# Optimization experiments

Measured on AMD Instinct MI355X. Metric: run time of the kernel, lower is better.

Reference implementation:

```python
import jax, jax.numpy as jnp
import numpy as np

K = 3  # number of propagation hops (matches init kwarg)
N = 50000
E = 800000
D = 96


def setup_inputs() -> dict:
    key = jax.random.key(0)
    k1, k2, k3, k4 = jax.random.split(key, 4)
    x = jax.random.normal(k1, (N, D), dtype=jnp.float32)
    edge_feature = jax.random.normal(k2, (E, D), dtype=jnp.float32)
    hopwise = jnp.ones((K + 1,), dtype=jnp.float32)  # nn.Parameter(torch.ones(K+1))
    edge_index = jax.random.randint(k3, (2, E), 0, N, dtype=jnp.int64)
    return {"x": x, "edge_feature": edge_feature, "hopwise": hopwise,
            "edge_index": edge_index}


def reference(x, edge_feature, hopwise, edge_index):
    row, col = edge_index[0], edge_index[1]
    n = x.shape[0]
    # degree of destination nodes (col), symmetric normalization
    deg = jax.ops.segment_sum(jnp.ones(col.shape, x.dtype), col, num_segments=n)
    deg_inv = jnp.where(deg > 0, jax.lax.rsqrt(jnp.maximum(deg, 1.0)) * jnp.where(deg > 0, 1.0, 0.0), 0.0)
    deg_inv = jnp.where(deg > 0, deg ** -0.5, 0.0)
    norm = (deg_inv[row] * deg_inv[col])[:, None]  # [E, 1]
    hidden = x * hopwise[0]
    for hop in range(K):
        # message: norm * (x_j + edge_feature); aggregate: scatter-add at col
        msg = norm * (x[row] + edge_feature)          # [E, D]
        x = jax.ops.segment_sum(msg, col, num_segments=n)  # [N, D]
        hidden = hidden + hopwise[hop + 1] * x
    return hidden
```

## Files before the change

### kernel.cpp

```cpp
#include <hip/hip_runtime.h>


#define CH 24
#define CH2 12

typedef float v4f __attribute__((ext_vector_type(4)));

__global__ void deg_kernel(const int* __restrict__ col, int* __restrict__ deg, int E) {
    int e = blockIdx.x * blockDim.x + threadIdx.x;
    if (e < E) atomicAdd(&deg[col[e]], 1);
}

__global__ void deginv_kernel(const int* __restrict__ deg, float* __restrict__ deginv, int n) {
    int i = blockIdx.x * blockDim.x + threadIdx.x;
    if (i < n) {
        int d = deg[i];
        deginv[i] = (d > 0) ? rsqrtf((float)d) : 0.0f;
    }
}

__global__ __launch_bounds__(256) void scan1_kernel(const int* __restrict__ deg,
                                                    int* __restrict__ starts,
                                                    int* __restrict__ bsums, int n) {
    int t = threadIdx.x;
    int i = blockIdx.x * 1024 + t * 4;
    int4 v = make_int4(0, 0, 0, 0);
    if (i + 3 < n) v = *(const int4*)(deg + i);
    else {
        if (i + 0 < n) v.x = deg[i + 0];
        if (i + 1 < n) v.y = deg[i + 1];
        if (i + 2 < n) v.z = deg[i + 2];
        if (i + 3 < n) v.w = deg[i + 3];
    }
    int s0 = v.x, s1 = s0 + v.y, s2 = s1 + v.z, s3 = s2 + v.w;
    int tot = s3;
    int lane = t & 63;
    int incl = tot;
    for (int off = 1; off < 64; off <<= 1) {
        int u = __shfl_up(incl, off, 64);
        if (lane >= off) incl += u;
    }
    __shared__ int wsum[4];
    __shared__ int woff[4];
    int wid = t >> 6;
    if (lane == 63) wsum[wid] = incl;
    __syncthreads();
    if (t == 0) { int a = 0; for (int w = 0; w < 4; ++w) { woff[w] = a; a += wsum[w]; } }
    __syncthreads();
    int excl = incl - tot + woff[wid];
    if (i + 0 < n) starts[i + 0] = excl;
    if (i + 1 < n) starts[i + 1] = excl + s0;
    if (i + 2 < n) starts[i + 2] = excl + s1;
    if (i + 3 < n) starts[i + 3] = excl + s2;
    if (t == 255) bsums[blockIdx.x] = woff[3] + wsum[3];
}

__global__ __launch_bounds__(64) void scan2_kernel(int* __restrict__ bsums, int nb,
                                                   int* __restrict__ starts, int n, int total) {
    int lane = threadIdx.x;
    int v = (lane < nb) ? bsums[lane] : 0;
    int incl = v;
    for (int off = 1; off < 64; off <<= 1) {
        int u = __shfl_up(incl, off, 64);
        if (lane >= off) incl += u;
    }
    if (lane < nb) bsums[lane] = incl - v;
    if (lane == 0) starts[n] = total;
}

__global__ __launch_bounds__(256) void scan3_kernel(int* __restrict__ starts,
                                                    int* __restrict__ cursor,
                                                    const int* __restrict__ bsums, int n) {
    int t = threadIdx.x;
    int i = blockIdx.x * 1024 + t * 4;
    int off = bsums[blockIdx.x];
    for (int k = 0; k < 4; ++k) {
        int ii = i + k;
        if (ii < n) {
            int s = starts[ii] + off;
            starts[ii] = s;
            cursor[ii] = s;
        }
    }
}

__global__ void fill_kernel(const int* __restrict__ col, const int* __restrict__ row,
                            const float* __restrict__ deginv, int* __restrict__ cursor,
                            int* __restrict__ eids, float2* __restrict__ edat, int E) {
    int e = blockIdx.x * blockDim.x + threadIdx.x;
    if (e < E) {
        int c = col[e], r = row[e];
        int pos = atomicAdd(&cursor[c], 1);
        eids[pos] = e;
        float2 o;
        o.x = __int_as_float(r);
        o.y = deginv[r] * deginv[c];
        edat[pos] = o;
    }
}

__global__ __launch_bounds__(256) void hop1_kernel(const int* __restrict__ starts,
                                                   const float2* __restrict__ edat,
                                                   const int* __restrict__ eids,
                                                   const float4* __restrict__ ef4,
                                                   const float4* __restrict__ x4,
                                                   float4* __restrict__ bvec4,
                                                   float4* __restrict__ xnext4,
                                                   float4* __restrict__ out4,
                                                   const float* __restrict__ hopwise,
                                                   int NC2) {
    int g = blockIdx.x * 256 + threadIdx.x;
    if (g >= NC2) return;
    int node = g / CH2;
    int c = g - node * CH2;
    int s = starts[node], e_end = starts[node + 1];
    float4 ab0 = make_float4(0.f, 0.f, 0.f, 0.f), ab1 = ab0;
    float4 ax0 = ab0, ax1 = ab0;
    int j = s;
    for (; j + 2 <= e_end; j += 2) {
        float2 a0 = edat[j], a1 = edat[j + 1];
        int e0 = eids[j], e1 = eids[j + 1];
        int r0 = __float_as_int(a0.x), r1 = __float_as_int(a1.x);
        const v4f* fp0 = (const v4f*)(ef4 + (size_t)e0 * CH + c);
        const v4f* fp1 = (const v4f*)(ef4 + (size_t)e1 * CH + c);
        const float4* xp0 = x4 + (size_t)r0 * CH + c;
        const float4* xp1 = x4 + (size_t)r1 * CH + c;
        v4f f00 = __builtin_nontemporal_load(fp0);
        v4f f01 = __builtin_nontemporal_load(fp0 + 12);
        v4f f10 = __builtin_nontemporal_load(fp1);
        v4f f11 = __builtin_nontemporal_load(fp1 + 12);
        float4 v00 = xp0[0], v01 = xp0[12];
        float4 v10 = xp1[0], v11 = xp1[12];
        ab0.x += a0.y * f00.x + a1.y * f10.x;
        ab0.y += a0.y * f00.y + a1.y * f10.y;
        ab0.z += a0.y * f00.z + a1.y * f10.z;
        ab0.w += a0.y * f00.w + a1.y * f10.w;
        ab1.x += a0.y * f01.x + a1.y * f11.x;
        ab1.y += a0.y * f01.y + a1.y * f11.y;
        ab1.z += a0.y * f01.z + a1.y * f11.z;
        ab1.w += a0.y * f01.w + a1.y * f11.w;
        ax0.x += a0.y * v00.x + a1.y * v10.x;
        ax0.y += a0.y * v00.y + a1.y * v10.y;
        ax0.z += a0.y * v00.z + a1.y * v10.z;
        ax0.w += a0.y * v00.w + a1.y * v10.w;
        ax1.x += a0.y * v01.x + a1.y * v11.x;
        ax1.y += a0.y * v01.y + a1.y * v11.y;
        ax1.z += a0.y * v01.z + a1.y * v11.z;
        ax1.w += a0.y * v01.w + a1.y * v11.w;
    }
    for (; j < e_end; ++j) {
        float2 a = edat[j];
        int e = eids[j];
        int r = __float_as_int(a.x);
        const v4f* fp = (const v4f*)(ef4 + (size_t)e * CH + c);
        const float4* xp = x4 + (size_t)r * CH + c;
        v4f f0 = __builtin_nontemporal_load(fp);
        v4f f1 = __builtin_nontemporal_load(fp + 12);
        float4 v0 = xp[0], v1 = xp[12];
        ab0.x += a.y * f0.x; ab0.y += a.y * f0.y; ab0.z += a.y * f0.z; ab0.w += a.y * f0.w;
        ab1.x += a.y * f1.x; ab1.y += a.y * f1.y; ab1.z += a.y * f1.z; ab1.w += a.y * f1.w;
        ax0.x += a.y * v0.x; ax0.y += a.y * v0.y; ax0.z += a.y * v0.z; ax0.w += a.y * v0.w;
        ax1.x += a.y * v1.x; ax1.y += a.y * v1.y; ax1.z += a.y * v1.z; ax1.w += a.y * v1.w;
    }
    float h0 = hopwise[0], h1 = hopwise[1];
    size_t o = (size_t)node * CH + c;
    float4 xs0 = x4[o], xs1 = x4[o + 12];
    float4 x10, x11;
    x10.x = ax0.x + ab0.x; x10.y = ax0.y + ab0.y; x10.z = ax0.z + ab0.z; x10.w = ax0.w + ab0.w;
    x11.x = ax1.x + ab1.x; x11.y = ax1.y + ab1.y; x11.z = ax1.z + ab1.z; x11.w = ax1.w + ab1.w;
    bvec4[o] = ab0; bvec4[o + 12] = ab1;
    xnext4[o] = x10; xnext4[o + 12] = x11;
    float4 ov0, ov1;
    ov0.x = h0 * xs0.x + h1 * x10.x; ov0.y = h0 * xs0.y + h1 * x10.y;
    ov0.z = h0 * xs0.z + h1 * x10.z; ov0.w = h0 * xs0.w + h1 * x10.w;
    ov1.x = h0 * xs1.x + h1 * x11.x; ov1.y = h0 * xs1.y + h1 * x11.y;
    ov1.z = h0 * xs1.z + h1 * x11.z; ov1.w = h0 * xs1.w + h1 * x11.w;
    out4[o] = ov0; out4[o + 12] = ov1;
}

__global__ __launch_bounds__(256) void hop_kernel(const int* __restrict__ starts,
                                                  const float2* __restrict__ edat,
                                                  const float4* __restrict__ xcur4,
                                                  const float4* __restrict__ bvec4,
                                                  float4* __restrict__ xnext4,
                                                  float4* __restrict__ out4,
                                                  const float* __restrict__ hopwise,
                                                  int hop, int writeNext, int NC2) {
    int g = blockIdx.x * 256 + threadIdx.x;
    if (g >= NC2) return;
    int node = g / CH2;
    int c = g - node * CH2;
    int s = starts[node], e_end = starts[node + 1];
    float4 ax0 = make_float4(0.f, 0.f, 0.f, 0.f), ax1 = ax0;
    int j = s;
    for (; j + 4 <= e_end; j += 4) {
        float2 a0 = edat[j], a1 = edat[j + 1], a2 = edat[j + 2], a3 = edat[j + 3];
        int r0 = __float_as_int(a0.x), r1 = __float_as_int(a1.x);
        int r2 = __float_as_int(a2.x), r3 = __float_as_int(a3.x);
        const float4* p0 = xcur4 + (size_t)r0 * CH + c;
        const float4* p1 = xcur4 + (size_t)r1 * CH + c;
        const float4* p2 = xcur4 + (size_t)r2 * CH + c;
        const float4* p3 = xcur4 + (size_t)r3 * CH + c;
        float4 v00 = p0[0], v01 = p0[12];
        float4 v10 = p1[0], v11 = p1[12];
        float4 v20 = p2[0], v21 = p2[12];
        float4 v30 = p3[0], v31 = p3[12];
        ax0.x += a0.y * v00.x + a1.y * v10.x + a2.y * v20.x + a3.y * v30.x;
        ax0.y += a0.y * v00.y + a1.y * v10.y + a2.y * v20.y + a3.y * v30.y;
        ax0.z += a0.y * v00.z + a1.y * v10.z + a2.y * v20.z + a3.y * v30.z;
        ax0.w += a0.y * v00.w + a1.y * v10.w + a2.y * v20.w + a3.y * v30.w;
        ax1.x += a0.y * v01.x + a1.y * v11.x + a2.y * v21.x + a3.y * v31.x;
        ax1.y += a0.y * v01.y + a1.y * v11.y + a2.y * v21.y + a3.y * v31.y;
        ax1.z += a0.y * v01.z + a1.y * v11.z + a2.y * v21.z + a3.y * v31.z;
        ax1.w += a0.y * v01.w + a1.y * v11.w + a2.y * v21.w + a3.y * v31.w;
    }
    for (; j < e_end; ++j) {
        float2 a = edat[j];
        int r = __float_as_int(a.x);
        const float4* p = xcur4 + (size_t)r * CH + c;
        float4 v0 = p[0], v1 = p[12];
        ax0.x += a.y * v0.x; ax0.y += a.y * v0.y; ax0.z += a.y * v0.z; ax0.w += a.y * v0.w;
        ax1.x += a.y * v1.x; ax1.y += a.y * v1.y; ax1.z += a.y * v1.z; ax1.w += a.y * v1.w;
    }
    float h = hopwise[hop];
    size_t o = (size_t)node * CH + c;
    float4 b0 = bvec4[o], b1 = bvec4[o + 12];
    float4 xv0, xv1;
    xv0.x = ax0.x + b0.x; xv0.y = ax0.y + b0.y; xv0.z = ax0.z + b0.z; xv0.w = ax0.w + b0.w;
    xv1.x = ax1.x + b1.x; xv1.y = ax1.y + b1.y; xv1.z = ax1.z + b1.z; xv1.w = ax1.w + b1.w;
    if (writeNext) { xnext4[o] = xv0; xnext4[o + 12] = xv1; }
    float4 ov0 = out4[o], ov1 = out4[o + 12];
    ov0.x += h * xv0.x; ov0.y += h * xv0.y; ov0.z += h * xv0.z; ov0.w += h * xv0.w;
    ov1.x += h * xv1.x; ov1.y += h * xv1.y; ov1.z += h * xv1.z; ov1.w += h * xv1.w;
    out4[o] = ov0; out4[o + 12] = ov1;
}

extern "C" void kernel_launch(void* const* d_in, const int* in_sizes, int n_in,
                              void* d_out, int out_size, void* d_ws, size_t ws_size,
                              hipStream_t stream) {
    const float* x       = (const float*)d_in[0];
    const float* ef      = (const float*)d_in[1];
    const float* hopwise = (const float*)d_in[2];
    const int*   eidx    = (const int*)d_in[3];

    const int E = in_sizes[3] / 2;
    const int D = in_sizes[1] / E;
    const int N = in_sizes[0] / D;
    const int K = in_sizes[2] - 1;
    const int NC2 = N * CH2;

    const int* row = eidx;
    const int* col = eidx + E;
    float* out = (float*)d_out;

    char* w = (char*)d_ws;
    int*    deg    = (int*)w;     w += (size_t)N * 4;
    int*    starts = (int*)w;     w += (size_t)(N + 8) * 4;
    int*    cursor = (int*)w;     w += (size_t)N * 4;
    int*    eids   = (int*)w;     w += (size_t)E * 4;
    float*  deginv = (float*)w;   w += (size_t)N * 4;
    int*    bsums  = (int*)w;     w += 256 * 4;
    float2* edat   = (float2*)w;  w += (size_t)E * 8;
    float*  bvec   = (float*)w;   w += (size_t)N * D * 4;
    float*  buf0   = (float*)w;   w += (size_t)N * D * 4;
    float*  buf1   = (float*)w;

    const int BT = 256;
    const int nScanBlocks = (N + 1023) / 1024;

    hipMemsetAsync(deg, 0, (size_t)N * sizeof(int), stream);
    deg_kernel<<<(E + BT - 1) / BT, BT, 0, stream>>>(col, deg, E);
    deginv_kernel<<<(N + BT - 1) / BT, BT, 0, stream>>>(deg, deginv, N);
    scan1_kernel<<<nScanBlocks, 256, 0, stream>>>(deg, starts, bsums, N);
    scan2_kernel<<<1, 64, 0, stream>>>(bsums, nScanBlocks, starts, N, E);
    scan3_kernel<<<nScanBlocks, 256, 0, stream>>>(starts, cursor, bsums, N);
    fill_kernel<<<(E + BT - 1) / BT, BT, 0, stream>>>(col, row, deginv, cursor, eids, edat, E);

    int hopBlocks = (NC2 + 255) / 256;
    hop1_kernel<<<hopBlocks, 256, 0, stream>>>(starts, edat, eids, (const float4*)ef,
                                               (const float4*)x, (float4*)bvec,
                                               (float4*)buf0, (float4*)out, hopwise, NC2);

    const float* xcur = buf0;
    for (int hop = 2; hop <= K; ++hop) {
        float* xnext = (hop & 1) ? buf1 : buf0;
        if (xnext == xcur) xnext = (xcur == buf0) ? buf1 : buf0;
        int writeNext = (hop < K) ? 1 : 0;
        hop_kernel<<<hopBlocks, 256, 0, stream>>>(starts, edat, (const float4*)xcur,
                                                  (const float4*)bvec, (float4*)xnext,
                                                  (float4*)out, hopwise, hop, writeNext, NC2);
        xcur = xnext;
    }
}
```

Baseline: 661.9 us.

## Split hop propagation into feature slabs with slab-major intermediate buffers

Edge-feature aggregation is split into its own kernel that computes bvec once. Each hop then runs as six launches, each covering a 16-float slab of the feature dimension, and the intermediate x buffers are stored slab-major. The aim is to keep each slab's gathered working set (about 3.2MB) resident in cache during the random gathers. In exchange, the CSR edge list is re-read six times per hop, launch count rises, and the first hop re-reads x with a strided layout.

Result: slower. 927.5 us (+40.1%).

```diff
diff --git a/kernel.cpp b/kernel.cpp
--- a/kernel.cpp
+++ b/kernel.cpp
@@ -2,9 +2,9 @@
 
 
 #define CH 24
-#define CH2 12
 
 typedef float v4f __attribute__((ext_vector_type(4)));
+typedef float v2f __attribute__((ext_vector_type(2)));
 
 __global__ void deg_kernel(const int* __restrict__ col, int* __restrict__ deg, int E) {
     int e = blockIdx.x * blockDim.x + threadIdx.x;
@@ -99,140 +99,104 @@
     }
 }
 
-__global__ __launch_bounds__(256) void hop1_kernel(const int* __restrict__ starts,
-                                                   const float2* __restrict__ edat,
-                                                   const int* __restrict__ eids,
-                                                   const float4* __restrict__ ef4,
-                                                   const float4* __restrict__ x4,
-                                                   float4* __restrict__ bvec4,
-                                                   float4* __restrict__ xnext4,
-                                                   float4* __restrict__ out4,
-                                                   const float* __restrict__ hopwise,
-                                                   int NC2) {
+__global__ __launch_bounds__(256) void b_kernel(const int* __restrict__ starts,
+                                                const float2* __restrict__ edat,
+                                                const int* __restrict__ eids,
+                                                const float4* __restrict__ ef4,
+                                                float4* __restrict__ bvec4,
+                                                int NC12) {
     int g = blockIdx.x * 256 + threadIdx.x;
-    if (g >= NC2) return;
-    int node = g / CH2;
-    int c = g - node * CH2;
+    if (g >= NC12) return;
+    int node = g / 12;
+    int c = g - node * 12;
     int s = starts[node], e_end = starts[node + 1];
-    float4 ab0 = make_float4(0.f, 0.f, 0.f, 0.f), ab1 = ab0;
-    float4 ax0 = ab0, ax1 = ab0;
+    v4f ab0 = (v4f)(0.f), ab1 = (v4f)(0.f);
     int j = s;
-    for (; j + 2 <= e_end; j += 2) {
-        float2 a0 = edat[j], a1 = edat[j + 1];
-        int e0 = eids[j], e1 = eids[j + 1];
-        int r0 = __float_as_int(a0.x), r1 = __float_as_int(a1.x);
-        const v4f* fp0 = (const v4f*)(ef4 + (size_t)e0 * CH + c);
-        const v4f* fp1 = (const v4f*)(ef4 + (size_t)e1 * CH + c);
-        const float4* xp0 = x4 + (size_t)r0 * CH + c;
-        const float4* xp1 = x4 + (size_t)r1 * CH + c;
-        v4f f00 = __builtin_nontemporal_load(fp0);
-        v4f f01 = __builtin_nontemporal_load(fp0 + 12);
-        v4f f10 = __builtin_nontemporal_load(fp1);
-        v4f f11 = __builtin_nontemporal_load(fp1 + 12);
-        float4 v00 = xp0[0], v01 = xp0[12];
-        float4 v10 = xp1[0], v11 = xp1[12];
-        ab0.x += a0.y * f00.x + a1.y * f10.x;
-        ab0.y += a0.y * f00.y + a1.y * f10.y;
-        ab0.z += a0.y * f00.z + a1.y * f10.z;
-        ab0.w += a0.y * f00.w + a1.y * f10.w;
-        ab1.x += a0.y * f01.x + a1.y * f11.x;
-        ab1.y += a0.y * f01.y + a1.y * f11.y;
-        ab1.z += a0.y * f01.z + a1.y * f11.z;
-        ab1.w += a0.y * f01.w + a1.y * f11.w;
-        ax0.x += a0.y * v00.x + a1.y * v10.x;
-        ax0.y += a0.y * v00.y + a1.y * v10.y;
-        ax0.z += a0.y * v00.z + a1.y * v10.z;
-        ax0.w += a0.y * v00.w + a1.y * v10.w;
-        ax1.x += a0.y * v01.x + a1.y * v11.x;
-        ax1.y += a0.y * v01.y + a1.y * v11.y;
-        ax1.z += a0.y * v01.z + a1.y * v11.z;
-        ax1.w += a0.y * v01.w + a1.y * v11.w;
+    for (; j + 4 <= e_end; j += 4) {
+        float2 a0 = edat[j], a1 = edat[j + 1], a2 = edat[j + 2], a3 = edat[j + 3];
+        int e0 = eids[j], e1 = eids[j + 1], e2 = eids[j + 2], e3 = eids[j + 3];
+        const v4f* p0 = (const v4f*)(ef4 + (size_t)e0 * CH + c);
+        const v4f* p1 = (const v4f*)(ef4 + (size_t)e1 * CH + c);
+        const v4f* p2 = (const v4f*)(ef4 + (size_t)e2 * CH + c);
+        const v4f* p3 = (const v4f*)(ef4 + (size_t)e3 * CH + c);
+        v4f f00 = __builtin_nontemporal_load(p0);
+        v4f f01 = __builtin_nontemporal_load(p0 + 12);
+        v4f f10 = __builtin_nontemporal_load(p1);
+        v4f f11 = __builtin_nontemporal_load(p1 + 12);
+        v4f f20 = __builtin_nontemporal_load(p2);
+        v4f f21 = __builtin_nontemporal_load(p2 + 12);
+        v4f f30 = __builtin_nontemporal_load(p3);
+        v4f f31 = __builtin_nontemporal_load(p3 + 12);
+        ab0 += a0.y * f00 + a1.y * f10 + a2.y * f20 + a3.y * f30;
+        ab1 += a0.y * f01 + a1.y * f11 + a2.y * f21 + a3.y * f31;
     }
     for (; j < e_end; ++j) {
         float2 a = edat[j];
         int e = eids[j];
-        int r = __float_as_int(a.x);
-        const v4f* fp = (const v4f*)(ef4 + (size_t)e * CH + c);
-        const float4* xp = x4 + (size_t)r * CH + c;
-        v4f f0 = __builtin_nontemporal_load(fp);
-        v4f f1 = __builtin_nontemporal_load(fp + 12);
-        float4 v0 = xp[0], v1 = xp[12];
-        ab0.x += a.y * f0.x; ab0.y += a.y * f0.y; ab0.z += a.y * f0.z; ab0.w += a.y * f0.w;
-        ab1.x += a.y * f1.x; ab1.y += a.y * f1.y; ab1.z += a.y * f1.z; ab1.w += a.y * f1.w;
-        ax0.x += a.y * v0.x; ax0.y += a.y * v0.y; ax0.z += a.y * v0.z; ax0.w += a.y * v0.w;
-        ax1.x += a.y * v1.x; ax1.y += a.y * v1.y; ax1.z += a.y * v1.z; ax1.w += a.y * v1.w;
-    }
-    float h0 = hopwise[0], h1 = hopwise[1];
-    size_t o = (size_t)node * CH + c;
-    float4 xs0 = x4[o], xs1 = x4[o + 12];
-    float4 x10, x11;
-    x10.x = ax0.x + ab0.x; x10.y = ax0.y + ab0.y; x10.z = ax0.z + ab0.z; x10.w = ax0.w + ab0.w;
-    x11.x = ax1.x + ab1.x; x11.y = ax1.y + ab1.y; x11.z = ax1.z + ab1.z; x11.w = ax1.w + ab1.w;
-    bvec4[o] = ab0; bvec4[o + 12] = ab1;
-    xnext4[o] = x10; xnext4[o + 12] = x11;
-    float4 ov0, ov1;
-    ov0.x = h0 * xs0.x + h1 * x10.x; ov0.y = h0 * xs0.y + h1 * x10.y;
-    ov0.z = h0 * xs0.z + h1 * x10.z; ov0.w = h0 * xs0.w + h1 * x10.w;
-    ov1.x = h0 * xs1.x + h1 * x11.x; ov1.y = h0 * xs1.y + h1 * x11.y;
-    ov1.z = h0 * xs1.z + h1 * x11.z; ov1.w = h0 * xs1.w + h1 * x11.w;
-    out4[o] = ov0; out4[o + 12] = ov1;
-}
-
-__global__ __launch_bounds__(256) void hop_kernel(const int* __restrict__ starts,
-                                                  const float2* __restrict__ edat,
-                                                  const float4* __restrict__ xcur4,
-                                                  const float4* __restrict__ bvec4,
-                                                  float4* __restrict__ xnext4,
-                                                  float4* __restrict__ out4,
-                                                  const float* __restrict__ hopwise,
-                                                  int hop, int writeNext, int NC2) {
+        const v4f* p = (const v4f*)(ef4 + (size_t)e * CH + c);
+        v4f f0 = __builtin_nontemporal_load(p);
+        v4f f1 = __builtin_nontemporal_load(p + 12);
+        ab0 += a.y * f0;
+        ab1 += a.y * f1;
+    }
+    v4f* bp = (v4f*)(bvec4 + (size_t)node * CH + c);
+    bp[0] = ab0;
+    bp[12] = ab1;
+}
+
+__global__ __launch_bounds__(256) void slab_kernel(const int* __restrict__ starts,
+                                                   const float2* __restrict__ edat,
+                                                   const float4* __restrict__ xprev4,
+                                                   int pstride,
+                                                   const float4* __restrict__ bvec4,
+                                                   float4* __restrict__ xnext4,
+                                                   int writeNext,
+                                                   float4* __restrict__ out4,
+                                                   const float* __restrict__ hopwise,
+                                                   int hop, int isFirst, int NC4) {
     int g = blockIdx.x * 256 + threadIdx.x;
-    if (g >= NC2) return;
-    int node = g / CH2;
-    int c = g - node * CH2;
+    if (g >= NC4) return;
+    int node = g >> 2;
+    int k = g & 3;
     int s = starts[node], e_end = starts[node + 1];
-    float4 ax0 = make_float4(0.f, 0.f, 0.f, 0.f), ax1 = ax0;
+    const v4f* xp = (const v4f*)xprev4;
+    v4f ax = (v4f)(0.f);
     int j = s;
     for (; j + 4 <= e_end; j += 4) {
-        float2 a0 = edat[j], a1 = edat[j + 1], a2 = edat[j + 2], a3 = edat[j + 3];
+        const v2f* ap = (const v2f*)(edat + j);
+        v2f a0 = __builtin_nontemporal_load(ap);
+        v2f a1 = __builtin_nontemporal_load(ap + 1);
+        v2f a2 = __builtin_nontemporal_load(ap + 2);
+        v2f a3 = __builtin_nontemporal_load(ap + 3);
         int r0 = __float_as_int(a0.x), r1 = __float_as_int(a1.x);
         int r2 = __float_as_int(a2.x), r3 = __float_as_int(a3.x);
-        const float4* p0 = xcur4 + (size_t)r0 * CH + c;
-        const float4* p1 = xcur4 + (size_t)r1 * CH + c;
-        const float4* p2 = xcur4 + (size_t)r2 * CH + c;
-        const float4* p3 = xcur4 + (size_t)r3 * CH + c;
-        float4 v00 = p0[0], v01 = p0[12];
-        float4 v10 = p1[0], v11 = p1[12];
-        float4 v20 = p2[0], v21 = p2[12];
-        float4 v30 = p3[0], v31 = p3[12];
-        ax0.x += a0.y * v00.x + a1.y * v10.x + a2.y * v20.x + a3.y * v30.x;
-        ax0.y += a0.y * v00.y + a1.y * v10.y + a2.y * v20.y + a3.y * v30.y;
-        ax0.z += a0.y * v00.z + a1.y * v10.z + a2.y * v20.z + a3.y * v30.z;
-        ax0.w += a0.y * v00.w + a1.y * v10.w + a2.y * v20.w + a3.y * v30.w;
-        ax1.x += a0.y * v01.x + a1.y * v11.x + a2.y * v21.x + a3.y * v31.x;
-        ax1.y += a0.y * v01.y + a1.y * v11.y + a2.y * v21.y + a3.y * v31.y;
-        ax1.z += a0.y * v01.z + a1.y * v11.z + a2.y * v21.z + a3.y * v31.z;
-        ax1.w += a0.y * v01.w + a1.y * v11.w + a2.y * v21.w + a3.y * v31.w;
+        v4f v0 = xp[(size_t)r0 * pstride + k];
+        v4f v1 = xp[(size_t)r1 * pstride + k];
+        v4f v2 = xp[(size_t)r2 * pstride + k];
+        v4f v3 = xp[(size_t)r3 * pstride + k];
+        ax += a0.y * v0 + a1.y * v1 + a2.y * v2 + a3.y * v3;
     }
     for (; j < e_end; ++j) {
-        float2 a = edat[j];
+        v2f a = __builtin_nontemporal_load((const v2f*)(edat + j));
         int r = __float_as_int(a.x);
-        const float4* p = xcur4 + (size_t)r * CH + c;
-        float4 v0 = p[0], v1 = p[12];
-        ax0.x += a.y * v0.x; ax0.y += a.y * v0.y; ax0.z += a.y * v0.z; ax0.w += a.y * v0.w;
-        ax1.x += a.y * v1.x; ax1.y += a.y * v1.y; ax1.z += a.y * v1.z; ax1.w += a.y * v1.w;
-    }
-    float h = hopwise[hop];
-    size_t o = (size_t)node * CH + c;
-    float4 b0 = bvec4[o], b1 = bvec4[o + 12];
-    float4 xv0, xv1;
-    xv0.x = ax0.x + b0.x; xv0.y = ax0.y + b0.y; xv0.z = ax0.z + b0.z; xv0.w = ax0.w + b0.w;
-    xv1.x = ax1.x + b1.x; xv1.y = ax1.y + b1.y; xv1.z = ax1.z + b1.z; xv1.w = ax1.w + b1.w;
-    if (writeNext) { xnext4[o] = xv0; xnext4[o + 12] = xv1; }
-    float4 ov0 = out4[o], ov1 = out4[o + 12];
-    ov0.x += h * xv0.x; ov0.y += h * xv0.y; ov0.z += h * xv0.z; ov0.w += h * xv0.w;
-    ov1.x += h * xv1.x; ov1.y += h * xv1.y; ov1.z += h * xv1.z; ov1.w += h * xv1.w;
-    out4[o] = ov0; out4[o + 12] = ov1;
+        ax += a.y * xp[(size_t)r * pstride + k];
+    }
+    size_t ob = (size_t)node * CH + k;
+    v4f b = __builtin_nontemporal_load((const v4f*)(bvec4 + ob));
+    v4f xv = ax + b;
+    if (writeNext)
+        __builtin_nontemporal_store(xv, (v4f*)(xnext4 + (size_t)node * 4 + k));
+    if (isFirst) {
+        float h0 = hopwise[0], h1 = hopwise[1];
+        v4f xs = xp[(size_t)node * pstride + k];
+        v4f ov = h0 * xs + h1 * xv;
+        __builtin_nontemporal_store(ov, (v4f*)(out4 + ob));
+    } else {
+        float h = hopwise[hop];
+        v4f ov = __builtin_nontemporal_load((const v4f*)(out4 + ob));
+        ov += h * xv;
+        __builtin_nontemporal_store(ov, (v4f*)(out4 + ob));
+    }
 }
 
 extern "C" void kernel_launch(void* const* d_in, const int* in_sizes, int n_in,
@@ -247,7 +211,9 @@
     const int D = in_sizes[1] / E;
     const int N = in_sizes[0] / D;
     const int K = in_sizes[2] - 1;
-    const int NC2 = N * CH2;
+    const int NSLAB = 6;
+    const int NC12 = N * 12;
+    const int NC4  = N * 4;
 
     const int* row = eidx;
     const int* col = eidx + E;
@@ -276,19 +242,32 @@
     scan3_kernel<<<nScanBlocks, 256, 0, stream>>>(starts, cursor, bsums, N);
     fill_kernel<<<(E + BT - 1) / BT, BT, 0, stream>>>(col, row, deginv, cursor, eids, edat, E);
 
-    int hopBlocks = (NC2 + 255) / 256;
-    hop1_kernel<<<hopBlocks, 256, 0, stream>>>(starts, edat, eids, (const float4*)ef,
-                                               (const float4*)x, (float4*)bvec,
-                                               (float4*)buf0, (float4*)out, hopwise, NC2);
-
+    b_kernel<<<(NC12 + 255) / 256, 256, 0, stream>>>(starts, edat, eids,
+                                                     (const float4*)ef, (float4*)bvec, NC12);
+
+    int slabBlocks = (NC4 + 255) / 256;
     const float* xcur = buf0;
-    for (int hop = 2; hop <= K; ++hop) {
-        float* xnext = (hop & 1) ? buf1 : buf0;
-        if (xnext == xcur) xnext = (xcur == buf0) ? buf1 : buf0;
+    for (int hop = 1; hop <= K; ++hop) {
+        const float* xprev;
+        int pstride;
+        float* xnext;
+        if (hop == 1) { xprev = x; pstride = CH; xnext = buf0; }
+        else {
+            xprev = xcur; pstride = 4;
+            xnext = (xcur == buf0) ? buf1 : buf0;
+        }
         int writeNext = (hop < K) ? 1 : 0;
-        hop_kernel<<<hopBlocks, 256, 0, stream>>>(starts, edat, (const float4*)xcur,
-                                                  (const float4*)bvec, (float4*)xnext,
-                                                  (float4*)out, hopwise, hop, writeNext, NC2);
-        xcur = xnext;
-    }
-}
+        for (int s = 0; s < NSLAB; ++s) {
+            const float4* xprev4 = (const float4*)xprev +
+                ((hop == 1) ? (size_t)s * 4 : (size_t)s * N * 4);
+            float4* xnext4 = (float4*)xnext + (size_t)s * N * 4;
+            slab_kernel<<<slabBlocks, 256, 0, stream>>>(
+                starts, edat, xprev4, pstride,
+                (const float4*)bvec + (size_t)s * 4,
+                xnext4, writeNext,
+                (float4*)out + (size_t)s * 4,
+                hopwise, hop, (hop == 1) ? 1 : 0, NC4);
+        }
+        if (hop >= 1) xcur = (hop == 1) ? buf0 : xnext;
+    }
+}
```
